# Kernel tuning notes

Hardware: AMD Instinct MI355X
Metric: run time of the kernel (lower is better)

## Reference

```python
import jax, jax.numpy as jnp
import numpy as np

DIM = 1024
HEADS = 16
HEAD_DIM = DIM // HEADS


def setup_inputs() -> dict:
    key = jax.random.key(0)
    ks = jax.random.split(key, 5)
    B, N = 4, 2048
    x = jax.random.normal(ks[0], (B, N, DIM), dtype=jnp.float32)
    # nn.Linear default init scale ~ 1/sqrt(fan_in)
    s = 1.0 / np.sqrt(DIM)
    W_qkv = jax.random.uniform(ks[1], (DIM, 3 * DIM), minval=-s, maxval=s, dtype=jnp.float32)
    b_qkv = jax.random.uniform(ks[2], (3 * DIM,), minval=-s, maxval=s, dtype=jnp.float32)
    W_proj = jax.random.uniform(ks[3], (DIM, DIM), minval=-s, maxval=s, dtype=jnp.float32)
    b_proj = jax.random.uniform(ks[4], (DIM,), minval=-s, maxval=s, dtype=jnp.float32)
    return {"x": x, "W_qkv": W_qkv, "b_qkv": b_qkv, "W_proj": W_proj, "b_proj": b_proj}


def reference(x, W_qkv, b_qkv, W_proj, b_proj):
    B, N, C = x.shape
    qkv = x @ W_qkv + b_qkv                      # [B, N, 3C]
    qkv = qkv.reshape(B, N, 3, HEADS, HEAD_DIM)
    q = jnp.transpose(qkv[:, :, 0], (0, 2, 1, 3))  # [B, H, N, D]
    k = jnp.transpose(qkv[:, :, 1], (0, 2, 1, 3))
    v = jnp.transpose(qkv[:, :, 2], (0, 2, 1, 3))
    scale = 1.0 / np.sqrt(HEAD_DIM)
    scores = jnp.einsum('bhqd,bhkd->bhqk', q, k) * scale  # [B, H, N, N]
    attn = jax.nn.softmax(scores, axis=-1)
    out = jnp.einsum('bhqk,bhkd->bhqd', attn, v)           # [B, H, N, D]
    out = jnp.transpose(out, (0, 2, 1, 3)).reshape(B, N, C)
    return out @ W_proj + b_proj
```

## Files before the change

kernel.cpp:

```cpp
#include <hip/hip_runtime.h>

typedef __attribute__((ext_vector_type(2)))  float  f32x2;
typedef __attribute__((ext_vector_type(4)))  float  f32x4;
typedef __attribute__((ext_vector_type(16))) float  f32x16;
typedef __attribute__((ext_vector_type(8)))  short  short8;
typedef __attribute__((ext_vector_type(4)))  unsigned int u32x4;
typedef __attribute__((ext_vector_type(2)))  unsigned int uint2v;

#define MFMA16 __builtin_amdgcn_mfma_f32_16x16x32_bf16
#define MFMA32 __builtin_amdgcn_mfma_f32_32x32x16_bf16

static __device__ __forceinline__ unsigned short f2bf(float f){
  union { float f; unsigned u; } v; v.f = f;
  unsigned r = v.u + 0x7fffu + ((v.u >> 16) & 1u);
  return (unsigned short)(r >> 16);
}

static __device__ __forceinline__ unsigned cvtpk(float a, float b){
  unsigned r;
  asm("v_cvt_pk_bf16_f32 %0, %1, %2" : "=v"(r) : "v"(a), "v"(b));
  return r;
}

static __device__ __forceinline__ void plswap(unsigned &a, unsigned &b){
  asm("v_permlane32_swap_b32 %0, %1" : "+v"(a), "+v"(b));
}

typedef __attribute__((address_space(1))) void gvoid_t;
typedef __attribute__((address_space(3))) void lvoid_t;

static __device__ __forceinline__ void gll16(const unsigned short* g, unsigned short* l){
  __builtin_amdgcn_global_load_lds((gvoid_t*)g, (lvoid_t*)l, 16, 0, 0);
}


__global__ __launch_bounds__(256) void k_prep(const float* __restrict__ x,
                                              unsigned short* __restrict__ xb,
                                              const float* __restrict__ Wq,
                                              unsigned short* __restrict__ Wqt,
                                              const float* __restrict__ Wp,
                                              unsigned short* __restrict__ Wpt){
  __shared__ __align__(16) unsigned char smraw[32768];
  const int bid = blockIdx.x, t = threadIdx.x;
  if (bid < 512){
    unsigned short* sm = (unsigned short*)smraw;
    const int mblk = bid >> 4, kt = bid & 15;
    const int l16 = t & 15, rg = t >> 4;
    #pragma unroll
    for (int p = 0; p < 16; p++){
      int row = p * 16 + rg;
      f32x4 v = *(const f32x4*)&x[(size_t)(mblk*256 + row) * 1024 + kt*64 + l16*4];
      uint2v u; u[0] = cvtpk(v[0], v[1]); u[1] = cvtpk(v[2], v[3]);
      int g = l16 >> 1;
      *(uint2v*)&sm[row*64 + ((g ^ (row & 7)) << 3) + (l16 & 1)*4] = u;
    }
    __syncthreads();
    size_t obase = (size_t)((mblk*16 + kt)*2) * 8192;
    #pragma unroll
    for (int i = 0; i < 8; i++){
      int o = i * 256 + t;
      int kh = o >> 10, rem = o & 1023;
      int band = rem >> 6, cc = (rem >> 4) & 3, ri = rem & 15;
      int r = band*16 + ri, g = kh*4 + cc;
      short8 vv = *(const short8*)&sm[r*64 + ((g ^ (r & 7)) << 3)];
      *(short8*)&xb[obase + (size_t)kh*8192 + rem*8] = vv;
    }
  } else {
    float (*tile)[33] = (float(*)[33])smraw;
    int wid = bid - 512;
    const float* W; unsigned short* Wt; int N, n0, k0;
    if (wid < 3072){ W = Wq; Wt = Wqt; N = 3072; n0 = (wid % 96)*32; k0 = (wid / 96)*32; }
    else { wid -= 3072; W = Wp; Wt = Wpt; N = 1024; n0 = (wid & 31)*32; k0 = (wid >> 5)*32; }
    const int tx = t & 31, ty = t >> 5;
    #pragma unroll
    for (int r = 0; r < 4; r++)
      tile[ty + 8*r][tx] = W[(size_t)(k0 + ty + 8*r) * N + n0 + tx];
    __syncthreads();
    #pragma unroll
    for (int r = 0; r < 4; r++){
      int nn = ty + 8*r;
      int n = n0 + nn, k = k0 + tx;
      int kt = k >> 6, kh = (k >> 5) & 1, cc = (k >> 3) & 3, ke = k & 7;
      int nblk = n >> 8, band = (n & 255) >> 4, ri = n & 15;
      Wt[(size_t)(((nblk*16 + kt)*2 + kh)) * 8192 + band*512 + cc*128 + ri*8 + ke] =
          f2bf(tile[tx][nn]);
    }
  }
}

#define VMW(N) { __builtin_amdgcn_sched_barrier(0);                        \
                 asm volatile("s_waitcnt vmcnt(" #N ")" ::: "memory");     \
                 __builtin_amdgcn_s_barrier();                             \
                 __builtin_amdgcn_sched_barrier(0); }

template<int MODE>
__global__ __launch_bounds__(512, 4) void k_gemm(const unsigned short* __restrict__ A,
                                                 const unsigned short* __restrict__ Bt,
                                                 const float* __restrict__ bias,
                                                 void* __restrict__ outp,
                                                 int NT){
  __shared__ __align__(16) unsigned short lds[36864];
  const int t = threadIdx.x, w = t >> 6, l = t & 63;
  const int wr = w >> 2, wc = w & 3;
  const int bx = blockIdx.x, by = blockIdx.y;
  const int mblk = bx >> 1, mhalf = bx & 1;

  const unsigned short* Ab = A + (size_t)mblk*262144 + mhalf*4096 + t*8;
  const unsigned short* Bb = Bt + (size_t)by*262144 + t*8;

  f32x4 acc[4][4];
  #pragma unroll
  for (int i = 0; i < 4; i++)
    #pragma unroll
    for (int j = 0; j < 4; j++)
      acc[i][j] = (f32x4){0.f, 0.f, 0.f, 0.f};

  auto stage = [&](int sl){
    const int b = sl % 3;
    const size_t off = (size_t)sl * 8192;
    gll16(Ab + off,        &lds[b*12288 + t*8]);
    gll16(Bb + off,        &lds[b*12288 + 4096 + t*8]);
    gll16(Bb + off + 4096, &lds[b*12288 + 8192 + t*8]);
  };

  auto phase = [&](int b, bool do_stage, int sl){
    short8 af[4], bfr[4];
    const int aoff = b*12288 + wr*2048 + l*8;
    const int boff = b*12288 + 4096 + wc*2048 + l*8;
    #pragma unroll
    for (int i = 0; i < 4; i++) af[i]  = *(const short8*)&lds[aoff + i*512];
    #pragma unroll
    for (int j = 0; j < 4; j++) bfr[j] = *(const short8*)&lds[boff + j*512];
    if (do_stage) stage(sl);
    __builtin_amdgcn_sched_barrier(0);
    __builtin_amdgcn_s_barrier();
    __builtin_amdgcn_s_setprio(1);
    #pragma unroll
    for (int i = 0; i < 4; i++)
      #pragma unroll
      for (int j = 0; j < 4; j++)
        acc[i][j] = MFMA16(af[i], bfr[j], acc[i][j], 0, 0, 0);
    __builtin_amdgcn_s_setprio(0);
  };

  stage(0); stage(1);
  VMW(3);

  const int NP = 2 * NT;
  int p = 0;
  for (; p <= NP - 3; ++p){
    phase(p % 3, true, p + 2);
    VMW(3);
  }
  phase(p % 3, false, 0); VMW(0); ++p;
  phase(p % 3, false, 0);

  if (MODE == 0){
    unsigned short* qg = (unsigned short*)outp;
    unsigned short* kg = qg + (size_t)8388608;
    unsigned short* vg = kg + (size_t)8388608;
    const int which = by >> 2;
    const int lrow = l & 15;
    #pragma unroll
    for (int j = 0; j < 4; j++){
      int col = by*256 + wc*64 + j*16 + lrow;
      float bi = bias[col];
      int cc = col & 1023;
      int h = cc >> 6;
      int d = j*16 + lrow;
      if (which == 2){
        int db = d >> 5, dd = d & 31;
        #pragma unroll
        for (int i = 0; i < 4; i++){
          int nn = bx*128 + wr*64 + i*16 + (l >> 4)*4;
          int b = nn >> 11, key = nn & 2047;
          size_t idx = (size_t)(key >> 6)*4096 + (size_t)(((key >> 4) & 3)*2 + db)*512
                     + (((key >> 3) & 1)*32 + dd)*8 + (key & 7);
          uint2v u;
          u[0] = cvtpk(acc[i][j][0] + bi, acc[i][j][1] + bi);
          u[1] = cvtpk(acc[i][j][2] + bi, acc[i][j][3] + bi);
          *(uint2v*)&vg[(size_t)(b*16 + h)*131072 + idx] = u;
        }
      } else {
        unsigned short* dst = which ? kg : qg;
        float scale = which ? 1.0f : 0.18033688011f;
        int dsub = (d >> 4)*512 + ((d >> 3) & 1)*256 + (d & 7);
        #pragma unroll
        for (int i = 0; i < 4; i++)
          #pragma unroll
          for (int reg = 0; reg < 4; reg++){
            int nn = bx*128 + wr*64 + i*16 + (l >> 4)*4 + reg;
            int b = nn >> 11, row = nn & 2047;
            dst[(size_t)(b*16 + h)*131072 + (size_t)(row >> 5)*2048 + dsub + (row & 31)*8] =
                f2bf((acc[i][j][reg] + bi) * scale);
          }
      }
    }
  } else {
    float* out = (float*)outp;
    #pragma unroll
    for (int i = 0; i < 4; i++)
      #pragma unroll
      for (int reg = 0; reg < 4; reg++){
        int row = bx*128 + wr*64 + i*16 + (l >> 4)*4 + reg;
        #pragma unroll
        for (int j = 0; j < 4; j++){
          int col = by*256 + wc*64 + j*16 + (l & 15);
          out[(size_t)row * 1024 + col] = acc[i][j][reg] + bias[col];
        }
      }
  }
}

__global__ __launch_bounds__(256, 2) void k_attn(const unsigned short* __restrict__ Qg,
                                                 const unsigned short* __restrict__ Kg,
                                                 const unsigned short* __restrict__ Vg,
                                                 unsigned short* __restrict__ aout){
  __shared__ __align__(16) unsigned short lds[20480];

  const int t = threadIdx.x, w = t >> 6, l = t & 63;
  const int hi = l >> 5, q31 = l & 31;
  const int d0 = blockIdx.x;
  const int xcd = d0 & 7, jj = d0 >> 3;
  const int bh = xcd + 8*(jj >> 3);
  const int bx = jj & 7;

  const unsigned short* Qp = Qg + (size_t)bh*131072 + (size_t)bx*16384;
  const unsigned short* Kp = Kg + (size_t)bh*131072;
  const unsigned short* Vp = Vg + (size_t)bh*131072;

  #pragma unroll
  for (int i = 0; i < 8; i++){ int c = i*256 + t; gll16(Qp + c*8, &lds[c*8]); }
  {
    short8 z8 = {0,0,0,0,0,0,0,0};
    *(short8*)&lds[16384 + t*16]     = z8;
    *(short8*)&lds[16384 + t*16 + 8] = z8;
  }
  __syncthreads();
  short8 qf0[4], qf1[4];
  #pragma unroll
  for (int ds = 0; ds < 4; ds++){
    qf0[ds] = *(const short8*)&lds[(2*w + 0)*2048 + ds*512 + l*8];
    qf1[ds] = *(const short8*)&lds[(2*w + 1)*2048 + ds*512 + l*8];
  }
  __syncthreads();

  #pragma unroll
  for (int i = 0; i < 2; i++){
    int c = i*256 + t;
    gll16(Kp + c*8, &lds[c*8]);
    gll16(Vp + c*8, &lds[8192 + c*8]);
  }
  __syncthreads();

  f32x16 ZERO;
  #pragma unroll
  for (int i = 0; i < 16; i++) ZERO[i] = 0.f;
  f32x16 o0lo = ZERO, o0hi = ZERO, o1lo = ZERO, o1hi = ZERO;
  float lsum0 = 0.f, lsum1 = 0.f;
  u32x4 pA0[4], pA1[4], pB0[4], pB1[4];
  #pragma unroll
  for (int ks = 0; ks < 4; ks++){
    pA0[ks][0]=0u; pA0[ks][1]=0u; pA0[ks][2]=0u; pA0[ks][3]=0u;
    pA1[ks][0]=0u; pA1[ks][1]=0u; pA1[ks][2]=0u; pA1[ks][3]=0u;
  }
  int s0 = 0, s1 = 1, s2 = 2;

  auto body = [&](int kt, u32x4 (&pO0)[4], u32x4 (&pO1)[4],
                          u32x4 (&pN0)[4], u32x4 (&pN1)[4]){
    const int cbk = (kt & 1) * 4096;
    if (kt < 31){
      const int nbk = cbk ^ 4096;
      const int nv  = 8192 + s1*4096;
      #pragma unroll
      for (int i = 0; i < 2; i++){
        int c = i*256 + t;
        gll16(Kp + (size_t)(kt + 1)*4096 + c*8, &lds[nbk + c*8]);
        gll16(Vp + (size_t)(kt + 1)*4096 + c*8, &lds[nv + c*8]);
      }
    }

    f32x16 sA0, sB0, sA1, sB1;
    __builtin_amdgcn_s_setprio(1);
    {
      short8 kfA = *(const short8*)&lds[cbk + l*8];
      short8 kfB = *(const short8*)&lds[cbk + 2048 + l*8];
      sA0 = MFMA32(kfA, qf0[0], ZERO, 0, 0, 0);
      sB0 = MFMA32(kfB, qf0[0], ZERO, 0, 0, 0);
      sA1 = MFMA32(kfA, qf1[0], ZERO, 0, 0, 0);
      sB1 = MFMA32(kfB, qf1[0], ZERO, 0, 0, 0);
    }
    #pragma unroll
    for (int ds = 1; ds < 4; ds++){
      short8 kfA = *(const short8*)&lds[cbk + ds*512 + l*8];
      short8 kfB = *(const short8*)&lds[cbk + 2048 + ds*512 + l*8];
      sA0 = MFMA32(kfA, qf0[ds], sA0, 0, 0, 0);
      sB0 = MFMA32(kfB, qf0[ds], sB0, 0, 0, 0);
      sA1 = MFMA32(kfA, qf1[ds], sA1, 0, 0, 0);
      sB1 = MFMA32(kfB, qf1[ds], sB1, 0, 0, 0);
    }
    __builtin_amdgcn_s_setprio(0);
    __builtin_amdgcn_sched_barrier(0);

    const int pvb = 8192 + s2*4096;

    #pragma unroll
    for (int i = 0; i < 16; i++){
      sA0[i] = __builtin_amdgcn_exp2f(sA0[i]);
      sB0[i] = __builtin_amdgcn_exp2f(sB0[i]);
      sA1[i] = __builtin_amdgcn_exp2f(sA1[i]);
      sB1[i] = __builtin_amdgcn_exp2f(sB1[i]);
    }
    lsum0 += ((((sA0[0]+sA0[1])+(sA0[2]+sA0[3])) + ((sA0[4]+sA0[5])+(sA0[6]+sA0[7])))
           +  (((sA0[8]+sA0[9])+(sA0[10]+sA0[11])) + ((sA0[12]+sA0[13])+(sA0[14]+sA0[15]))))
           + ((((sB0[0]+sB0[1])+(sB0[2]+sB0[3])) + ((sB0[4]+sB0[5])+(sB0[6]+sB0[7])))
           +  (((sB0[8]+sB0[9])+(sB0[10]+sB0[11])) + ((sB0[12]+sB0[13])+(sB0[14]+sB0[15]))));
    lsum1 += ((((sA1[0]+sA1[1])+(sA1[2]+sA1[3])) + ((sA1[4]+sA1[5])+(sA1[6]+sA1[7])))
           +  (((sA1[8]+sA1[9])+(sA1[10]+sA1[11])) + ((sA1[12]+sA1[13])+(sA1[14]+sA1[15]))))
           + ((((sB1[0]+sB1[1])+(sB1[2]+sB1[3])) + ((sB1[4]+sB1[5])+(sB1[6]+sB1[7])))
           +  (((sB1[8]+sB1[9])+(sB1[10]+sB1[11])) + ((sB1[12]+sB1[13])+(sB1[14]+sB1[15]))));

    {
      unsigned wA[8], wB[8];
      #pragma unroll
      for (int j = 0; j < 8; j++){ wA[j] = cvtpk(sA0[2*j], sA0[2*j+1]); wB[j] = cvtpk(sB0[2*j], sB0[2*j+1]); }
      { unsigned a=wA[0],b=wA[2]; plswap(a,b); pN0[0][0]=a; pN0[0][2]=b; }
      { unsigned a=wA[1],b=wA[3]; plswap(a,b); pN0[0][1]=a; pN0[0][3]=b; }
      { unsigned a=wA[4],b=wA[6]; plswap(a,b); pN0[1][0]=a; pN0[1][2]=b; }
      { unsigned a=wA[5],b=wA[7]; plswap(a,b); pN0[1][1]=a; pN0[1][3]=b; }
      { unsigned a=wB[0],b=wB[2]; plswap(a,b); pN0[2][0]=a; pN0[2][2]=b; }
      { unsigned a=wB[1],b=wB[3]; plswap(a,b); pN0[2][1]=a; pN0[2][3]=b; }
      { unsigned a=wB[4],b=wB[6]; plswap(a,b); pN0[3][0]=a; pN0[3][2]=b; }
      { unsigned a=wB[5],b=wB[7]; plswap(a,b); pN0[3][1]=a; pN0[3][3]=b; }
    }
    {
      unsigned wA[8], wB[8];
      #pragma unroll
      for (int j = 0; j < 8; j++){ wA[j] = cvtpk(sA1[2*j], sA1[2*j+1]); wB[j] = cvtpk(sB1[2*j], sB1[2*j+1]); }
      { unsigned a=wA[0],b=wA[2]; plswap(a,b); pN1[0][0]=a; pN1[0][2]=b; }
      { unsigned a=wA[1],b=wA[3]; plswap(a,b); pN1[0][1]=a; pN1[0][3]=b; }
      { unsigned a=wA[4],b=wA[6]; plswap(a,b); pN1[1][0]=a; pN1[1][2]=b; }
      { unsigned a=wA[5],b=wA[7]; plswap(a,b); pN1[1][1]=a; pN1[1][3]=b; }
      { unsigned a=wB[0],b=wB[2]; plswap(a,b); pN1[2][0]=a; pN1[2][2]=b; }
      { unsigned a=wB[1],b=wB[3]; plswap(a,b); pN1[2][1]=a; pN1[2][3]=b; }
      { unsigned a=wB[4],b=wB[6]; plswap(a,b); pN1[3][0]=a; pN1[3][2]=b; }
      { unsigned a=wB[5],b=wB[7]; plswap(a,b); pN1[3][1]=a; pN1[3][3]=b; }
    }

    #pragma unroll
    for (int ks = 0; ks < 4; ks++){
      short8 p0r, p1r;
      *(u32x4*)&p0r = pO0[ks];
      *(u32x4*)&p1r = pO1[ks];
      short8 vf0 = *(const short8*)&lds[pvb + (ks*2 + 0)*512 + l*8];
      short8 vf1 = *(const short8*)&lds[pvb + (ks*2 + 1)*512 + l*8];
      o0lo = MFMA32(vf0, p0r, o0lo, 0, 0, 0);
      o0hi = MFMA32(vf1, p0r, o0hi, 0, 0, 0);
      o1lo = MFMA32(vf0, p1r, o1lo, 0, 0, 0);
      o1hi = MFMA32(vf1, p1r, o1hi, 0, 0, 0);
    }

    #pragma unroll
    for (int g4 = 0; g4 < 4; g4++){
      __builtin_amdgcn_sched_group_barrier(0x100, 2, 0);
      __builtin_amdgcn_sched_group_barrier(0x002, 40, 0);
      __builtin_amdgcn_sched_group_barrier(0x008, 4, 0);
    }
    __builtin_amdgcn_sched_group_barrier(0x002, 64, 0);

    __syncthreads();
    int tmp = s2; s2 = s0; s0 = s1; s1 = tmp;
  };

  for (int kt2 = 0; kt2 < 32; kt2 += 2){
    body(kt2,     pA0, pA1, pB0, pB1);
    body(kt2 + 1, pB0, pB1, pA0, pA1);
  }

  {
    const int pvb = 8192 + s2*4096;
    __builtin_amdgcn_s_setprio(1);
    #pragma unroll
    for (int ks = 0; ks < 4; ks++){
      short8 p0r, p1r;
      *(u32x4*)&p0r = pA0[ks];
      *(u32x4*)&p1r = pA1[ks];
      short8 vf0 = *(const short8*)&lds[pvb + (ks*2 + 0)*512 + l*8];
      short8 vf1 = *(const short8*)&lds[pvb + (ks*2 + 1)*512 + l*8];
      o0lo = MFMA32(vf0, p0r, o0lo, 0, 0, 0);
      o0hi = MFMA32(vf1, p0r, o0hi, 0, 0, 0);
      o1lo = MFMA32(vf0, p1r, o1lo, 0, 0, 0);
      o1hi = MFMA32(vf1, p1r, o1hi, 0, 0, 0);
    }
    __builtin_amdgcn_s_setprio(0);
  }
  __syncthreads();

  lsum0 += __shfl_xor(lsum0, 32);
  lsum1 += __shfl_xor(lsum1, 32);
  {
    float inv0 = 1.0f / lsum0, inv1 = 1.0f / lsum1;
    int qr0 = w*64 + q31, qr1 = w*64 + 32 + q31;
    #pragma unroll
    for (int j = 0; j < 8; j++){
      int dd0 = 8*(j >> 1) + 2*(j & 1) + 4*hi;
      int dd1 = dd0 + 32;
      *(unsigned*)&lds[qr0*64 + (((dd0 >> 3) ^ (qr0 & 7)) << 3) + (dd0 & 7)] =
          cvtpk(o0lo[2*j] * inv0, o0lo[2*j+1] * inv0);
      *(unsigned*)&lds[qr0*64 + (((dd1 >> 3) ^ (qr0 & 7)) << 3) + (dd1 & 7)] =
          cvtpk(o0hi[2*j] * inv0, o0hi[2*j+1] * inv0);
      *(unsigned*)&lds[qr1*64 + (((dd0 >> 3) ^ (qr1 & 7)) << 3) + (dd0 & 7)] =
          cvtpk(o1lo[2*j] * inv1, o1lo[2*j+1] * inv1);
      *(unsigned*)&lds[qr1*64 + (((dd1 >> 3) ^ (qr1 & 7)) << 3) + (dd1 & 7)] =
          cvtpk(o1hi[2*j] * inv1, o1hi[2*j+1] * inv1);
    }
  }
  __syncthreads();
  {
    int mblk = (bh >> 4)*8 + bx;
    int h = bh & 15;
    #pragma unroll
    for (int i = 0; i < 8; i++){
      int idx = i*256 + t;
      int kh = idx >> 10, rem = idx & 1023;
      int band = rem >> 6, cc = (rem >> 4) & 3, ri = rem & 15;
      int r = band*16 + ri, g = kh*4 + cc;
      short8 vv = *(const short8*)&lds[r*64 + ((g ^ (r & 7)) << 3)];
      size_t chunk = (size_t)((mblk*16 + h)*2 + kh);
      *(short8*)&aout[chunk*8192 + (size_t)band*512 + cc*128 + ri*8] = vv;
    }
  }
}

extern "C" void kernel_launch(void* const* d_in, const int* in_sizes, int n_in,
                              void* d_out, int out_size, void* d_ws, size_t ws_size,
                              hipStream_t stream){
  const float* x     = (const float*)d_in[0];
  const float* Wqkv  = (const float*)d_in[1];
  const float* bqkv  = (const float*)d_in[2];
  const float* Wproj = (const float*)d_in[3];
  const float* bproj = (const float*)d_in[4];

  unsigned short* ws   = (unsigned short*)d_ws;
  unsigned short* xb   = ws;
  unsigned short* Wqt  = ws + (size_t)8192 * 1024;
  unsigned short* Wpt  = Wqt + (size_t)3072 * 1024;
  unsigned short* qkvb = Wpt + (size_t)1024 * 1024;

  k_prep<<<4608, 256, 0, stream>>>(x, xb, Wqkv, Wqt, Wproj, Wpt);
  k_gemm<0><<<dim3(64, 12), 512, 0, stream>>>(xb, Wqt, bqkv, qkvb, 16);
  k_attn<<<512, 256, 0, stream>>>(qkvb, qkvb + (size_t)8388608,
                                  qkvb + (size_t)16777216, xb);
  k_gemm<1><<<dim3(64, 4), 512, 0, stream>>>(xb, Wpt, bproj, (void*)d_out, 16);
}
```

Measured before the change: 155.0 us.

## Compute softmax row sums via MFMA and retile output projection GEMM

The attention kernel no longer sums the exponentiated scores with scalar VALU adds. It runs extra MFMAs that multiply a ones matrix by the packed bf16 probabilities, which accumulates the row sums on the matrix cores and removes the final cross-lane shuffle. The scheduling group hints are adjusted to match the smaller VALU count. Separately, the output projection GEMM becomes its own kernel with a 128x128 tile, which doubles the grid to 512 blocks for better CU occupancy. The new row sums are taken from bf16-rounded probabilities, which slightly changes numerics, and the extra MFMAs add matrix-core work.

New measurement: 166.7 us. 1.08x slower.

```diff
diff --git a/kernel.cpp b/kernel.cpp
--- a/kernel.cpp
+++ b/kernel.cpp
@@ -93,12 +93,11 @@
                  __builtin_amdgcn_s_barrier();                             \
                  __builtin_amdgcn_sched_barrier(0); }
 
-template<int MODE>
-__global__ __launch_bounds__(512, 4) void k_gemm(const unsigned short* __restrict__ A,
-                                                 const unsigned short* __restrict__ Bt,
-                                                 const float* __restrict__ bias,
-                                                 void* __restrict__ outp,
-                                                 int NT){
+__global__ __launch_bounds__(512, 4) void k_gemm0(const unsigned short* __restrict__ A,
+                                                  const unsigned short* __restrict__ Bt,
+                                                  const float* __restrict__ bias,
+                                                  unsigned short* __restrict__ qg,
+                                                  int NT){
   __shared__ __align__(16) unsigned short lds[36864];
   const int t = threadIdx.x, w = t >> 6, l = t & 63;
   const int wr = w >> 2, wc = w & 3;
@@ -155,61 +154,117 @@
   phase(p % 3, false, 0); VMW(0); ++p;
   phase(p % 3, false, 0);
 
-  if (MODE == 0){
-    unsigned short* qg = (unsigned short*)outp;
-    unsigned short* kg = qg + (size_t)8388608;
-    unsigned short* vg = kg + (size_t)8388608;
-    const int which = by >> 2;
-    const int lrow = l & 15;
-    #pragma unroll
-    for (int j = 0; j < 4; j++){
-      int col = by*256 + wc*64 + j*16 + lrow;
-      float bi = bias[col];
-      int cc = col & 1023;
-      int h = cc >> 6;
-      int d = j*16 + lrow;
-      if (which == 2){
-        int db = d >> 5, dd = d & 31;
+  unsigned short* kg = qg + (size_t)8388608;
+  unsigned short* vg = kg + (size_t)8388608;
+  const int which = by >> 2;
+  const int lrow = l & 15;
+  #pragma unroll
+  for (int j = 0; j < 4; j++){
+    int col = by*256 + wc*64 + j*16 + lrow;
+    float bi = bias[col];
+    int cc = col & 1023;
+    int h = cc >> 6;
+    int d = j*16 + lrow;
+    if (which == 2){
+      int db = d >> 5, dd = d & 31;
+      #pragma unroll
+      for (int i = 0; i < 4; i++){
+        int nn = bx*128 + wr*64 + i*16 + (l >> 4)*4;
+        int b = nn >> 11, key = nn & 2047;
+        size_t idx = (size_t)(key >> 6)*4096 + (size_t)(((key >> 4) & 3)*2 + db)*512
+                   + (((key >> 3) & 1)*32 + dd)*8 + (key & 7);
+        uint2v u;
+        u[0] = cvtpk(acc[i][j][0] + bi, acc[i][j][1] + bi);
+        u[1] = cvtpk(acc[i][j][2] + bi, acc[i][j][3] + bi);
+        *(uint2v*)&vg[(size_t)(b*16 + h)*131072 + idx] = u;
+      }
+    } else {
+      unsigned short* dst = which ? kg : qg;
+      float scale = which ? 1.0f : 0.18033688011f;
+      int dsub = (d >> 4)*512 + ((d >> 3) & 1)*256 + (d & 7);
+      #pragma unroll
+      for (int i = 0; i < 4; i++)
         #pragma unroll
-        for (int i = 0; i < 4; i++){
-          int nn = bx*128 + wr*64 + i*16 + (l >> 4)*4;
-          int b = nn >> 11, key = nn & 2047;
-          size_t idx = (size_t)(key >> 6)*4096 + (size_t)(((key >> 4) & 3)*2 + db)*512
-                     + (((key >> 3) & 1)*32 + dd)*8 + (key & 7);
-          uint2v u;
-          u[0] = cvtpk(acc[i][j][0] + bi, acc[i][j][1] + bi);
-          u[1] = cvtpk(acc[i][j][2] + bi, acc[i][j][3] + bi);
-          *(uint2v*)&vg[(size_t)(b*16 + h)*131072 + idx] = u;
+        for (int reg = 0; reg < 4; reg++){
+          int nn = bx*128 + wr*64 + i*16 + (l >> 4)*4 + reg;
+          int b = nn >> 11, row = nn & 2047;
+          dst[(size_t)(b*16 + h)*131072 + (size_t)(row >> 5)*2048 + dsub + (row & 31)*8] =
+              f2bf((acc[i][j][reg] + bi) * scale);
         }
-      } else {
-        unsigned short* dst = which ? kg : qg;
-        float scale = which ? 1.0f : 0.18033688011f;
-        int dsub = (d >> 4)*512 + ((d >> 3) & 1)*256 + (d & 7);
-        #pragma unroll
-        for (int i = 0; i < 4; i++)
-          #pragma unroll
-          for (int reg = 0; reg < 4; reg++){
-            int nn = bx*128 + wr*64 + i*16 + (l >> 4)*4 + reg;
-            int b = nn >> 11, row = nn & 2047;
-            dst[(size_t)(b*16 + h)*131072 + (size_t)(row >> 5)*2048 + dsub + (row & 31)*8] =
-                f2bf((acc[i][j][reg] + bi) * scale);
-          }
+    }
+  }
+}
+
+__global__ __launch_bounds__(512, 4) void k_gemmP(const unsigned short* __restrict__ A,
+                                                  const unsigned short* __restrict__ Bt,
+                                                  const float* __restrict__ bias,
+                                                  float* __restrict__ out,
+                                                  int NT){
+  __shared__ __align__(16) unsigned short lds[24576];
+  const int t = threadIdx.x, w = t >> 6, l = t & 63;
+  const int wr = w >> 2, wc = w & 3;
+  const int bx = blockIdx.x, by = blockIdx.y;
+
+  const unsigned short* Ab = A + (size_t)(bx >> 1)*262144 + (bx & 1)*4096 + t*8;
+  const unsigned short* Bb = Bt + (size_t)(by >> 1)*262144 + (by & 1)*4096 + t*8;
+
+  f32x4 acc[4][2];
+  #pragma unroll
+  for (int i = 0; i < 4; i++)
+    #pragma unroll
+    for (int j = 0; j < 2; j++)
+      acc[i][j] = (f32x4){0.f, 0.f, 0.f, 0.f};
+
+  auto stage = [&](int sl){
+    const int b = sl % 3;
+    const size_t off = (size_t)sl * 8192;
+    gll16(Ab + off, &lds[b*8192 + t*8]);
+    gll16(Bb + off, &lds[b*8192 + 4096 + t*8]);
+  };
+
+  auto phase = [&](int b, bool do_stage, int sl){
+    short8 af[4], bfr[2];
+    const int aoff = b*8192 + wr*2048 + l*8;
+    const int boff = b*8192 + 4096 + wc*1024 + l*8;
+    #pragma unroll
+    for (int i = 0; i < 4; i++) af[i]  = *(const short8*)&lds[aoff + i*512];
+    #pragma unroll
+    for (int j = 0; j < 2; j++) bfr[j] = *(const short8*)&lds[boff + j*512];
+    if (do_stage) stage(sl);
+    __builtin_amdgcn_sched_barrier(0);
+    __builtin_amdgcn_s_barrier();
+    __builtin_amdgcn_s_setprio(1);
+    #pragma unroll
+    for (int i = 0; i < 4; i++)
+      #pragma unroll
+      for (int j = 0; j < 2; j++)
+        acc[i][j] = MFMA16(af[i], bfr[j], acc[i][j], 0, 0, 0);
+    __builtin_amdgcn_s_setprio(0);
+  };
+
+  stage(0); stage(1);
+  VMW(2);
+
+  const int NP = 2 * NT;
+  int p = 0;
+  for (; p <= NP - 3; ++p){
+    phase(p % 3, true, p + 2);
+    VMW(2);
+  }
+  phase(p % 3, false, 0); VMW(0); ++p;
+  phase(p % 3, false, 0);
+
+  #pragma unroll
+  for (int i = 0; i < 4; i++)
+    #pragma unroll
+    for (int reg = 0; reg < 4; reg++){
+      int row = bx*128 + wr*64 + i*16 + (l >> 4)*4 + reg;
+      #pragma unroll
+      for (int j = 0; j < 2; j++){
+        int col = by*128 + wc*32 + j*16 + (l & 15);
+        out[(size_t)row * 1024 + col] = acc[i][j][reg] + bias[col];
       }
     }
-  } else {
-    float* out = (float*)outp;
-    #pragma unroll
-    for (int i = 0; i < 4; i++)
-      #pragma unroll
-      for (int reg = 0; reg < 4; reg++){
-        int row = bx*128 + wr*64 + i*16 + (l >> 4)*4 + reg;
-        #pragma unroll
-        for (int j = 0; j < 4; j++){
-          int col = by*256 + wc*64 + j*16 + (l & 15);
-          out[(size_t)row * 1024 + col] = acc[i][j][reg] + bias[col];
-        }
-      }
-  }
 }
 
 __global__ __launch_bounds__(256, 2) void k_attn(const unsigned short* __restrict__ Qg,
@@ -257,7 +312,8 @@
   #pragma unroll
   for (int i = 0; i < 16; i++) ZERO[i] = 0.f;
   f32x16 o0lo = ZERO, o0hi = ZERO, o1lo = ZERO, o1hi = ZERO;
-  float lsum0 = 0.f, lsum1 = 0.f;
+  f32x16 lsC0 = ZERO, lsC1 = ZERO;
+  const short8 ONES = {0x3F80,0x3F80,0x3F80,0x3F80,0x3F80,0x3F80,0x3F80,0x3F80};
   u32x4 pA0[4], pA1[4], pB0[4], pB1[4];
   #pragma unroll
   for (int ks = 0; ks < 4; ks++){
@@ -311,14 +367,6 @@
       sA1[i] = __builtin_amdgcn_exp2f(sA1[i]);
       sB1[i] = __builtin_amdgcn_exp2f(sB1[i]);
     }
-    lsum0 += ((((sA0[0]+sA0[1])+(sA0[2]+sA0[3])) + ((sA0[4]+sA0[5])+(sA0[6]+sA0[7])))
-           +  (((sA0[8]+sA0[9])+(sA0[10]+sA0[11])) + ((sA0[12]+sA0[13])+(sA0[14]+sA0[15]))))
-           + ((((sB0[0]+sB0[1])+(sB0[2]+sB0[3])) + ((sB0[4]+sB0[5])+(sB0[6]+sB0[7])))
-           +  (((sB0[8]+sB0[9])+(sB0[10]+sB0[11])) + ((sB0[12]+sB0[13])+(sB0[14]+sB0[15]))));
-    lsum1 += ((((sA1[0]+sA1[1])+(sA1[2]+sA1[3])) + ((sA1[4]+sA1[5])+(sA1[6]+sA1[7])))
-           +  (((sA1[8]+sA1[9])+(sA1[10]+sA1[11])) + ((sA1[12]+sA1[13])+(sA1[14]+sA1[15]))))
-           + ((((sB1[0]+sB1[1])+(sB1[2]+sB1[3])) + ((sB1[4]+sB1[5])+(sB1[6]+sB1[7])))
-           +  (((sB1[8]+sB1[9])+(sB1[10]+sB1[11])) + ((sB1[12]+sB1[13])+(sB1[14]+sB1[15]))));
 
     {
       unsigned wA[8], wB[8];
@@ -345,6 +393,15 @@
       { unsigned a=wB[1],b=wB[3]; plswap(a,b); pN1[2][1]=a; pN1[2][3]=b; }
       { unsigned a=wB[4],b=wB[6]; plswap(a,b); pN1[3][0]=a; pN1[3][2]=b; }
       { unsigned a=wB[5],b=wB[7]; plswap(a,b); pN1[3][1]=a; pN1[3][3]=b; }
+    }
+
+    #pragma unroll
+    for (int ks = 0; ks < 4; ks++){
+      short8 pn0, pn1;
+      *(u32x4*)&pn0 = pN0[ks];
+      *(u32x4*)&pn1 = pN1[ks];
+      lsC0 = MFMA32(ONES, pn0, lsC0, 0, 0, 0);
+      lsC1 = MFMA32(ONES, pn1, lsC1, 0, 0, 0);
     }
 
     #pragma unroll
@@ -363,10 +420,10 @@
     #pragma unroll
     for (int g4 = 0; g4 < 4; g4++){
       __builtin_amdgcn_sched_group_barrier(0x100, 2, 0);
-      __builtin_amdgcn_sched_group_barrier(0x002, 40, 0);
-      __builtin_amdgcn_sched_group_barrier(0x008, 4, 0);
-    }
-    __builtin_amdgcn_sched_group_barrier(0x002, 64, 0);
+      __builtin_amdgcn_sched_group_barrier(0x002, 28, 0);
+      __builtin_amdgcn_sched_group_barrier(0x008, 6, 0);
+    }
+    __builtin_amdgcn_sched_group_barrier(0x002, 48, 0);
 
     __syncthreads();
     int tmp = s2; s2 = s0; s0 = s1; s1 = tmp;
@@ -396,10 +453,8 @@
   }
   __syncthreads();
 
-  lsum0 += __shfl_xor(lsum0, 32);
-  lsum1 += __shfl_xor(lsum1, 32);
   {
-    float inv0 = 1.0f / lsum0, inv1 = 1.0f / lsum1;
+    float inv0 = 1.0f / lsC0[0], inv1 = 1.0f / lsC1[0];
     int qr0 = w*64 + q31, qr1 = w*64 + 32 + q31;
     #pragma unroll
     for (int j = 0; j < 8; j++){
@@ -448,8 +503,8 @@
   unsigned short* qkvb = Wpt + (size_t)1024 * 1024;
 
   k_prep<<<4608, 256, 0, stream>>>(x, xb, Wqkv, Wqt, Wproj, Wpt);
-  k_gemm<0><<<dim3(64, 12), 512, 0, stream>>>(xb, Wqt, bqkv, qkvb, 16);
+  k_gemm0<<<dim3(64, 12), 512, 0, stream>>>(xb, Wqt, bqkv, qkvb, 16);
   k_attn<<<512, 256, 0, stream>>>(qkvb, qkvb + (size_t)8388608,
                                   qkvb + (size_t)16777216, xb);
-  k_gemm<1><<<dim3(64, 4), 512, 0, stream>>>(xb, Wpt, bproj, (void*)d_out, 16);
-}
+  k_gemmP<<<dim3(64, 8), 512, 0, stream>>>(xb, Wpt, bproj, (float*)d_out, 16);
+}
```
